# Kernel optimization log

Measured on AMD Instinct MI355X. Metric: run time of the kernel, lower is better.

## Reference

```python
import jax, jax.numpy as jnp
import numpy as np

N_NODES = 20000
N_GRAPHS = 8
NODES_PER_GRAPH = N_NODES // N_GRAPHS
DEG = 16
N_EDGES = N_NODES * DEG
D = 128
MAX_ITER = 8
HISTORY = 5
LAM = 0.1
LN_EPS = 1e-5


def setup_inputs() -> dict:
    key = jax.random.key(0)
    k1, k2, k3, k4, k5 = jax.random.split(key, 5)
    # edges constrained to stay within each graph's node block
    src = jax.random.randint(k1, (N_EDGES,), 0, N_NODES, dtype=jnp.int32)
    offs = (src // NODES_PER_GRAPH) * NODES_PER_GRAPH
    dst = offs + jax.random.randint(k2, (N_EDGES,), 0, NODES_PER_GRAPH, dtype=jnp.int32)
    # scale values ~1/deg so the fixed-point map stays well-behaved
    sparse_values = jax.random.normal(k3, (N_EDGES,), dtype=jnp.float32) * (1.0 / DEG)
    return {
        "x_init": jax.random.normal(k4, (N_NODES, D), dtype=jnp.float32),
        "norm_K_diag": jax.random.uniform(k5, (N_NODES, 1), dtype=jnp.float32),
        "sparse_values": sparse_values,
        "ln_w": jnp.ones((D,), dtype=jnp.float32),
        "ln_b": jnp.zeros((D,), dtype=jnp.float32),
        "edge_rows": src,
        "edge_cols": dst,
        "batch": jnp.repeat(jnp.arange(N_GRAPHS, dtype=jnp.int32), NODES_PER_GRAPH),
        "max_iter": MAX_ITER,
    }


def _spmm(vals, rows, cols, z):
    # sparse COO matmul: out[r] += vals_e * z[cols_e]; coalesce-equivalent since
    # segment_sum adds duplicate indices.
    return jax.ops.segment_sum(vals[:, None] * z[cols], rows, num_segments=N_NODES)


def _layernorm(x, w, b):
    mu = jnp.mean(x, axis=-1, keepdims=True)
    var = jnp.mean((x - mu) ** 2, axis=-1, keepdims=True)
    return w * (x - mu) * jax.lax.rsqrt(var + LN_EPS) + b


def reference(x_init, norm_K_diag, sparse_values, ln_w, ln_b, edge_rows, edge_cols, batch, max_iter):
    def f(z):
        out = norm_K_diag * z + _spmm(sparse_values, edge_rows, edge_cols, z)
        return _layernorm(out, ln_w, ln_b)

    z = x_init
    z_hist, f_hist = [], []
    for i in range(max_iter):  # fixed, small unroll (DEQ max_iter)
        f_z = f(z)
        z_hist.append(z.reshape(-1))
        f_hist.append(f_z.reshape(-1))
        if len(z_hist) > HISTORY:
            z_hist.pop(0)
            f_hist.pop(0)
        if len(z_hist) > 1 and i > 5:
            Z = jnp.stack(z_hist, axis=1)   # [N*D, h]
            F = jnp.stack(f_hist, axis=1)
            G = F - Z
            dG = G[:, 1:] - G[:, :-1]
            dF = F[:, 1:] - F[:, :-1]
            H = dG.T @ dG + LAM * jnp.eye(dG.shape[1], dtype=z.dtype)
            gamma = jnp.linalg.solve(H, dG.T @ G[:, -1:])
            z_new = (F[:, -1:] - dF @ gamma).reshape(z.shape)
            z = jnp.where(jnp.all(jnp.isfinite(z_new)), 0.5 * f_z + 0.5 * z_new, f_z)
        else:
            z = f_z
    return z
```

## Files before the change

### kernel.cpp

```cpp
#include <hip/hip_runtime.h>
#include <math.h>

#define N_NODES 20000
#define N_EDGES 320000
#define DD 128
#define ND (N_NODES * DD)
#define ND4 (ND / 4)
#define NPG 2500


__global__ void count_kernel(const int* __restrict__ rows, int* __restrict__ cnt) {
    int e = blockIdx.x * blockDim.x + threadIdx.x;
    if (e < N_EDGES) atomicAdd(&cnt[rows[e]], 1);
}

__global__ __launch_bounds__(1024) void scan_kernel(const int* __restrict__ cnt,
                                                    int* __restrict__ row_start,
                                                    int* __restrict__ cursor,
                                                    float* __restrict__ redz) {
    const int t = threadIdx.x;
    if (t < 448) redz[t] = 0.0f;
    __shared__ int part[1024];
    const int CH = (N_NODES + 1023) / 1024;
    int lo = t * CH, hi = min(lo + CH, N_NODES);
    int s = 0;
    for (int i = lo; i < hi; ++i) s += cnt[i];
    part[t] = s;
    __syncthreads();
    for (int off = 1; off < 1024; off <<= 1) {
        int v = (t >= off) ? part[t - off] : 0;
        __syncthreads();
        if (t >= off) part[t] += v;
        __syncthreads();
    }
    int run = (t > 0) ? part[t - 1] : 0;
    for (int i = lo; i < hi; ++i) {
        row_start[i] = run;
        cursor[i] = run;
        run += cnt[i];
    }
    if (t == 1023) row_start[N_NODES] = part[1023];
}

__global__ void scatter_kernel(const int* __restrict__ rows, const int* __restrict__ cols,
                               const float* __restrict__ vals, int* __restrict__ cursor,
                               float2* __restrict__ epack) {
    int e = blockIdx.x * blockDim.x + threadIdx.x;
    if (e >= N_EDGES) return;
    int r = rows[e];
    int p = atomicAdd(&cursor[r], 1);
    epack[p] = make_float2(vals[e], __int_as_float(cols[e]));
}


__global__ __launch_bounds__(128) void feval_kernel(const float* __restrict__ z,
                                                    const float* __restrict__ Kd,
                                                    const float* __restrict__ lnw,
                                                    const float* __restrict__ lnb,
                                                    const int* __restrict__ row_start,
                                                    const float2* __restrict__ epack,
                                                    float* __restrict__ out) {
    int b = blockIdx.x;
    int g = b & 7;
    int j = b >> 3;
    int wv = threadIdx.x >> 6;
    int lane = threadIdx.x & 63;
    int l = lane & 31;
    int r = g * NPG + (j << 2) + (wv << 1) + (lane >> 5);
    int d0 = l << 2;

    int e0 = row_start[r], e1 = row_start[r + 1];

    float4 zv = *(const float4*)(z + (size_t)r * DD + d0);
    float kd = Kd[r];
    float a0 = kd * zv.x, a1 = kd * zv.y, a2 = kd * zv.z, a3 = kd * zv.w;

    int e = e0;
    for (; e + 8 <= e1; e += 8) {
        float2 ep[8];
#pragma unroll
        for (int u = 0; u < 8; ++u) ep[u] = epack[e + u];
        float4 zr[8];
#pragma unroll
        for (int u = 0; u < 8; ++u)
            zr[u] = *(const float4*)(z + (size_t)__float_as_int(ep[u].y) * DD + d0);
#pragma unroll
        for (int u = 0; u < 8; ++u) {
            float v = ep[u].x;
            a0 = fmaf(v, zr[u].x, a0); a1 = fmaf(v, zr[u].y, a1);
            a2 = fmaf(v, zr[u].z, a2); a3 = fmaf(v, zr[u].w, a3);
        }
    }
    for (; e < e1; ++e) {
        float2 ep = epack[e];
        float4 zc = *(const float4*)(z + (size_t)__float_as_int(ep.y) * DD + d0);
        float v = ep.x;
        a0 = fmaf(v, zc.x, a0); a1 = fmaf(v, zc.y, a1);
        a2 = fmaf(v, zc.z, a2); a3 = fmaf(v, zc.w, a3);
    }

    float s = a0 + a1 + a2 + a3;
    float sq = a0 * a0 + a1 * a1 + a2 * a2 + a3 * a3;
#pragma unroll
    for (int off = 16; off; off >>= 1) {
        s += __shfl_xor(s, off, 64);
        sq += __shfl_xor(sq, off, 64);
    }
    float mu = s * (1.0f / DD);
    float var = sq * (1.0f / DD) - mu * mu;
    float rstd = rsqrtf(var + 1e-5f);

    float4 wv4 = *(const float4*)(lnw + d0);
    float4 bv4 = *(const float4*)(lnb + d0);
    float4 ov;
    ov.x = wv4.x * (a0 - mu) * rstd + bv4.x;
    ov.y = wv4.y * (a1 - mu) * rstd + bv4.y;
    ov.z = wv4.z * (a2 - mu) * rstd + bv4.z;
    ov.w = wv4.w * (a3 - mu) * rstd + bv4.w;
    *(float4*)(out + (size_t)r * DD + d0) = ov;
}


struct Slots { const float* s[6]; const float* zlast; };
struct Cols5 { const float* f[5]; };

__device__ __forceinline__ float dot4(float4 a, float4 b) {
    return a.x * b.x + a.y * b.y + a.z * b.z + a.w * b.w;
}
__device__ __forceinline__ float4 sub4(float4 a, float4 b) {
    return make_float4(a.x - b.x, a.y - b.y, a.z - b.z, a.w - b.w);
}

#define RED_T 160000
__global__ __launch_bounds__(256) void reduce_kernel(Slots sl, float* __restrict__ red) {
    int tid = blockIdx.x * 256 + threadIdx.x;
    float acc[14];
#pragma unroll
    for (int k = 0; k < 14; ++k) acc[k] = 0.f;

#pragma unroll
    for (int ph = 0; ph < 2; ++ph) {
        int ja = tid + (2 * ph) * RED_T;
        int jb = ja + RED_T;
        float4 fa[6], fb[6];
#pragma unroll
        for (int c = 0; c < 6; ++c) {
            fa[c] = ((const float4*)sl.s[c])[ja];
            fb[c] = ((const float4*)sl.s[c])[jb];
        }
        float4 zla = ((const float4*)sl.zlast)[ja];
        float4 zlb = ((const float4*)sl.zlast)[jb];
        float4 Ga[5], Gb[5];
#pragma unroll
        for (int c = 0; c < 4; ++c) { Ga[c] = sub4(fa[c + 1], fa[c]); Gb[c] = sub4(fb[c + 1], fb[c]); }
        Ga[4] = sub4(fa[5], zla);
        Gb[4] = sub4(fb[5], zlb);
        float4 dga[4], dgb[4];
#pragma unroll
        for (int a = 0; a < 4; ++a) { dga[a] = sub4(Ga[a + 1], Ga[a]); dgb[a] = sub4(Gb[a + 1], Gb[a]); }
        int k = 0;
#pragma unroll
        for (int a = 0; a < 4; ++a)
#pragma unroll
            for (int b = a; b < 4; ++b) { acc[k] += dot4(dga[a], dga[b]) + dot4(dgb[a], dgb[b]); ++k; }
#pragma unroll
        for (int a = 0; a < 4; ++a) acc[10 + a] += dot4(dga[a], Ga[4]) + dot4(dgb[a], Gb[4]);
    }

#pragma unroll
    for (int off = 32; off; off >>= 1)
#pragma unroll
        for (int kk = 0; kk < 14; ++kk) acc[kk] += __shfl_xor(acc[kk], off, 64);

    __shared__ float sh[4][14];
    int wave = threadIdx.x >> 6, lane = threadIdx.x & 63;
    if (lane == 0)
#pragma unroll
        for (int kk = 0; kk < 14; ++kk) sh[wave][kk] = acc[kk];
    __syncthreads();
    if (threadIdx.x < 14) {
        int kk = threadIdx.x;
        atomicAdd(&red[kk * 16], sh[0][kk] + sh[1][kk] + sh[2][kk] + sh[3][kk]);
    }
}

__device__ __forceinline__ float solve_gamma(const float* __restrict__ red, float* g) {
    float A[4][4], b[4];
    int k = 0;
#pragma unroll
    for (int a = 0; a < 4; ++a)
#pragma unroll
        for (int c = 0; c < 4; ++c) A[a][c] = 0.f;
#pragma unroll
    for (int a = 0; a < 4; ++a)
#pragma unroll
        for (int c = a; c < 4; ++c) { float h = red[k * 16]; A[a][c] = h; A[c][a] = h; ++k; }
#pragma unroll
    for (int a = 0; a < 4; ++a) A[a][a] += 0.1f;
#pragma unroll
    for (int a = 0; a < 4; ++a) b[a] = red[(10 + a) * 16];

#pragma unroll
    for (int col = 0; col < 4; ++col) {
        float inv = 1.0f / A[col][col];
#pragma unroll
        for (int rr = 0; rr < 4; ++rr) {
            if (rr > col) {
                float m = A[rr][col] * inv;
#pragma unroll
                for (int c2 = 0; c2 < 4; ++c2)
                    if (c2 >= col) A[rr][c2] -= m * A[col][c2];
                b[rr] -= m * b[col];
            }
        }
    }
#pragma unroll
    for (int rr = 3; rr >= 0; --rr) {
        float s = b[rr];
#pragma unroll
        for (int c2 = 0; c2 < 4; ++c2)
            if (c2 > rr) s -= A[rr][c2] * g[c2];
        g[rr] = s / A[rr][rr];
    }
    bool fin = isfinite(g[0]) && isfinite(g[1]) && isfinite(g[2]) && isfinite(g[3]);
    return fin ? 1.0f : 0.0f;
}

__global__ __launch_bounds__(256) void update_kernel(Cols5 c, const float* __restrict__ red,
                                                     float* __restrict__ zout) {
    int j = blockIdx.x * blockDim.x + threadIdx.x;
    if (j >= ND4) return;
    float g[4];
    float flag = solve_gamma(red, g);
    float g0 = g[0], g1 = g[1], g2 = g[2], g3 = g[3];
    float4 f0 = ((const float4*)c.f[0])[j];
    float4 f1 = ((const float4*)c.f[1])[j];
    float4 f2 = ((const float4*)c.f[2])[j];
    float4 f3 = ((const float4*)c.f[3])[j];
    float4 f4 = ((const float4*)c.f[4])[j];
    float4 o;
    if (flag != 0.0f) {
        o.x = f4.x - 0.5f * ((f1.x - f0.x) * g0 + (f2.x - f1.x) * g1 + (f3.x - f2.x) * g2 + (f4.x - f3.x) * g3);
        o.y = f4.y - 0.5f * ((f1.y - f0.y) * g0 + (f2.y - f1.y) * g1 + (f3.y - f2.y) * g2 + (f4.y - f3.y) * g3);
        o.z = f4.z - 0.5f * ((f1.z - f0.z) * g0 + (f2.z - f1.z) * g1 + (f3.z - f2.z) * g2 + (f4.z - f3.z) * g3);
        o.w = f4.w - 0.5f * ((f1.w - f0.w) * g0 + (f2.w - f1.w) * g1 + (f3.w - f2.w) * g2 + (f4.w - f3.w) * g3);
    } else {
        o = f4;
    }
    ((float4*)zout)[j] = o;
}


extern "C" void kernel_launch(void* const* d_in, const int* in_sizes, int n_in,
                              void* d_out, int out_size, void* d_ws, size_t ws_size,
                              hipStream_t stream) {
    const float* x_init = (const float*)d_in[0];
    const float* Kd     = (const float*)d_in[1];
    const float* vals   = (const float*)d_in[2];
    const float* lnw    = (const float*)d_in[3];
    const float* lnb    = (const float*)d_in[4];
    const int*   rows   = (const int*)d_in[5];
    const int*   cols   = (const int*)d_in[6];
    float* out = (float*)d_out;

    char* p = (char*)d_ws;
    auto carve = [&](size_t bytes) -> void* {
        void* r = (void*)p;
        p += (bytes + 255) & ~(size_t)255;
        return r;
    };
    float*  Fh        = (float*)carve((size_t)6 * ND * 4);
    float*  red       = (float*)carve(4096);
    int*    row_start = (int*)carve((N_NODES + 1) * 4);
    int*    cursor    = (int*)carve(N_NODES * 4);
    int*    cnt       = (int*)carve(N_NODES * 4);
    float2* epack     = (float2*)carve((size_t)N_EDGES * 8);
    float*  zA        = out;

    hipMemsetAsync(cnt, 0, N_NODES * 4, stream);
    count_kernel<<<(N_EDGES + 255) / 256, 256, 0, stream>>>(rows, cnt);
    scan_kernel<<<1, 1024, 0, stream>>>(cnt, row_start, cursor, red);
    scatter_kernel<<<(N_EDGES + 255) / 256, 256, 0, stream>>>(rows, cols, vals, cursor, epack);

    auto Fslot = [&](int t) -> float* { return Fh + (size_t)(t % 6) * ND; };

    for (int t = 0; t < 8; ++t) {
        const float* zsrc = (t == 0) ? x_init : (t <= 6 ? Fslot(t - 1) : zA);
        feval_kernel<<<5000, 128, 0, stream>>>(zsrc, Kd, lnw, lnb, row_start, epack, Fslot(t));

        if (t >= 6) {
            float* redt = red + (t - 6) * 224;
            Slots sl;
            for (int i = 0; i < 6; ++i) sl.s[i] = Fslot(t - 5 + i);
            sl.zlast = (t == 7) ? (const float*)zA : (const float*)Fslot(t - 1);
            reduce_kernel<<<625, 256, 0, stream>>>(sl, redt);

            Cols5 uc;
            for (int c2 = 0; c2 < 5; ++c2) uc.f[c2] = Fslot(t - 4 + c2);
            float* zdst = (t == 6) ? zA : out;
            update_kernel<<<(ND4 + 255) / 256, 256, 0, stream>>>(uc, redt, zdst);
        }
    }
}
```

Before: 334.1 us.

## Map one wave per row and broadcast edge metadata via readlane in SpMM

Rewrites the SpMM+LayerNorm kernel so each 64-lane wave handles a whole row, with each lane owning two feature columns instead of four. The wave loads up to 64 edge (val, col) pairs cooperatively in one coalesced load and broadcasts them with readlane, replacing per-lane redundant loads of the packed edge list. Blocks grow to 256 threads (4 rows each). The aim is less redundant edge-metadata traffic and more parallelism per row. The cost is narrower float2 gathers and a serial readlane loop that keeps only 4 gathers in flight instead of 8.

New measurement: 338.8 us. Within noise of the previous version (+1.4%).

```diff
diff --git a/kernel.cpp b/kernel.cpp
--- a/kernel.cpp
+++ b/kernel.cpp
@@ -53,7 +53,7 @@
 }
 
 
-__global__ __launch_bounds__(128) void feval_kernel(const float* __restrict__ z,
+__global__ __launch_bounds__(256) void feval_kernel(const float* __restrict__ z,
                                                     const float* __restrict__ Kd,
                                                     const float* __restrict__ lnw,
                                                     const float* __restrict__ lnb,
@@ -63,46 +63,54 @@
     int b = blockIdx.x;
     int g = b & 7;
     int j = b >> 3;
-    int wv = threadIdx.x >> 6;
+    int wave = threadIdx.x >> 6;
     int lane = threadIdx.x & 63;
-    int l = lane & 31;
-    int r = g * NPG + (j << 2) + (wv << 1) + (lane >> 5);
-    int d0 = l << 2;
+    int r = g * NPG + (j << 2) + wave;
+    int d0 = lane << 1;
 
     int e0 = row_start[r], e1 = row_start[r + 1];
 
-    float4 zv = *(const float4*)(z + (size_t)r * DD + d0);
+    float2 zv = *(const float2*)(z + (size_t)r * DD + d0);
     float kd = Kd[r];
-    float a0 = kd * zv.x, a1 = kd * zv.y, a2 = kd * zv.z, a3 = kd * zv.w;
-
-    int e = e0;
-    for (; e + 8 <= e1; e += 8) {
-        float2 ep[8];
-#pragma unroll
-        for (int u = 0; u < 8; ++u) ep[u] = epack[e + u];
-        float4 zr[8];
-#pragma unroll
-        for (int u = 0; u < 8; ++u)
-            zr[u] = *(const float4*)(z + (size_t)__float_as_int(ep[u].y) * DD + d0);
-#pragma unroll
-        for (int u = 0; u < 8; ++u) {
-            float v = ep[u].x;
-            a0 = fmaf(v, zr[u].x, a0); a1 = fmaf(v, zr[u].y, a1);
-            a2 = fmaf(v, zr[u].z, a2); a3 = fmaf(v, zr[u].w, a3);
-        }
-    }
-    for (; e < e1; ++e) {
-        float2 ep = epack[e];
-        float4 zc = *(const float4*)(z + (size_t)__float_as_int(ep.y) * DD + d0);
-        float v = ep.x;
-        a0 = fmaf(v, zc.x, a0); a1 = fmaf(v, zc.y, a1);
-        a2 = fmaf(v, zc.z, a2); a3 = fmaf(v, zc.w, a3);
-    }
-
-    float s = a0 + a1 + a2 + a3;
-    float sq = a0 * a0 + a1 * a1 + a2 * a2 + a3 * a3;
-#pragma unroll
-    for (int off = 16; off; off >>= 1) {
+    float a0 = kd * zv.x, a1 = kd * zv.y;
+
+    for (int base = e0; base < e1; base += 64) {
+        int ew = base + lane;
+        float2 my_e = (ew < e1) ? epack[ew] : make_float2(0.0f, 0.0f);
+        int my_col = __float_as_int(my_e.y);
+        int my_vali = __float_as_int(my_e.x);
+        int m = min(64, e1 - base);
+        int i = 0;
+        for (; i + 4 <= m; i += 4) {
+            int c0 = __builtin_amdgcn_readlane(my_col, i);
+            int c1 = __builtin_amdgcn_readlane(my_col, i + 1);
+            int c2 = __builtin_amdgcn_readlane(my_col, i + 2);
+            int c3 = __builtin_amdgcn_readlane(my_col, i + 3);
+            float v0 = __uint_as_float(__builtin_amdgcn_readlane(my_vali, i));
+            float v1 = __uint_as_float(__builtin_amdgcn_readlane(my_vali, i + 1));
+            float v2 = __uint_as_float(__builtin_amdgcn_readlane(my_vali, i + 2));
+            float v3 = __uint_as_float(__builtin_amdgcn_readlane(my_vali, i + 3));
+            float2 z0 = *(const float2*)(z + (size_t)c0 * DD + d0);
+            float2 z1 = *(const float2*)(z + (size_t)c1 * DD + d0);
+            float2 z2 = *(const float2*)(z + (size_t)c2 * DD + d0);
+            float2 z3 = *(const float2*)(z + (size_t)c3 * DD + d0);
+            a0 = fmaf(v0, z0.x, a0); a1 = fmaf(v0, z0.y, a1);
+            a0 = fmaf(v1, z1.x, a0); a1 = fmaf(v1, z1.y, a1);
+            a0 = fmaf(v2, z2.x, a0); a1 = fmaf(v2, z2.y, a1);
+            a0 = fmaf(v3, z3.x, a0); a1 = fmaf(v3, z3.y, a1);
+        }
+        for (; i < m; ++i) {
+            int c = __builtin_amdgcn_readlane(my_col, i);
+            float v = __uint_as_float(__builtin_amdgcn_readlane(my_vali, i));
+            float2 zc = *(const float2*)(z + (size_t)c * DD + d0);
+            a0 = fmaf(v, zc.x, a0); a1 = fmaf(v, zc.y, a1);
+        }
+    }
+
+    float s = a0 + a1;
+    float sq = a0 * a0 + a1 * a1;
+#pragma unroll
+    for (int off = 32; off; off >>= 1) {
         s += __shfl_xor(s, off, 64);
         sq += __shfl_xor(sq, off, 64);
     }
@@ -110,14 +118,12 @@
     float var = sq * (1.0f / DD) - mu * mu;
     float rstd = rsqrtf(var + 1e-5f);
 
-    float4 wv4 = *(const float4*)(lnw + d0);
-    float4 bv4 = *(const float4*)(lnb + d0);
-    float4 ov;
-    ov.x = wv4.x * (a0 - mu) * rstd + bv4.x;
-    ov.y = wv4.y * (a1 - mu) * rstd + bv4.y;
-    ov.z = wv4.z * (a2 - mu) * rstd + bv4.z;
-    ov.w = wv4.w * (a3 - mu) * rstd + bv4.w;
-    *(float4*)(out + (size_t)r * DD + d0) = ov;
+    float2 w2 = *(const float2*)(lnw + d0);
+    float2 b2 = *(const float2*)(lnb + d0);
+    float2 ov;
+    ov.x = w2.x * (a0 - mu) * rstd + b2.x;
+    ov.y = w2.y * (a1 - mu) * rstd + b2.y;
+    *(float2*)(out + (size_t)r * DD + d0) = ov;
 }
 
 
@@ -286,7 +292,7 @@
 
     for (int t = 0; t < 8; ++t) {
         const float* zsrc = (t == 0) ? x_init : (t <= 6 ? Fslot(t - 1) : zA);
-        feval_kernel<<<5000, 128, 0, stream>>>(zsrc, Kd, lnw, lnb, row_start, epack, Fslot(t));
+        feval_kernel<<<5000, 256, 0, stream>>>(zsrc, Kd, lnw, lnb, row_start, epack, Fslot(t));
 
         if (t >= 6) {
             float* redt = red + (t - 6) * 224;
```
